# Performance work log

Hardware: AMD Instinct MI355X
Metric: run time of the kernel (lower is better)

## Reference

```python
import jax, jax.numpy as jnp
import numpy as np

BATCH, LENGTH, IN, STATE, OUT = 8, 4096, 512, 256, 512


def setup_inputs() -> dict:
    key = jax.random.key(0)
    k1, k2, k3, k4, k5 = jax.random.split(key, 5)
    u = jax.random.normal(k1, (BATCH, LENGTH, IN), dtype=jnp.float32)
    x0 = jax.random.normal(k2, (BATCH, STATE), dtype=jnp.float32)
    A = 0.9999 * (2.0 * jax.random.uniform(k3, (STATE,), dtype=jnp.float32) - 1.0)
    B = jax.random.normal(k4, (IN, STATE), dtype=jnp.float32) / (STATE + IN) ** 0.5
    C = jax.random.normal(k5, (STATE, OUT), dtype=jnp.float32) / STATE ** 0.5
    return {"u": u, "x0": x0, "A": A, "B": B, "C": C}


def reference(u, x0, A, B, C):
    L = u.shape[1]
    # A_powers[t, n] = A[n] ** t, shape [L, state]
    A_powers = jnp.power(A[None, :], jnp.arange(L, dtype=u.dtype)[:, None])
    uB = u @ B  # [batch, L, state]
    # FFT convolution; inputs are real so rfft/irfft gives same result as
    # real(ifft(fft*fft)) in the original.
    T = 2 ** int(np.ceil(np.log2(2 * L - 1)))
    Af = jnp.fft.rfft(A_powers, n=T, axis=0)  # [T/2+1, state]
    Uf = jnp.fft.rfft(uB, n=T, axis=1)        # [batch, T/2+1, state]
    x = jnp.fft.irfft(Af[None, :, :] * Uf, n=T, axis=1)[:, :L]  # [batch, L, state]
    # initial-state contribution: A * A_powers * x0
    x = x + A[None, None, :] * A_powers[None, :, :] * x0[:, None, :]
    y = x @ C  # [batch, L, out]
    return (y, x[:, -1])
```

## Files before the change

kernel.cpp:

```cpp
#include <hip/hip_runtime.h>

#define BATCH   8
#define LENGTH  4096
#define IN_DIM  512
#define STATE   256
#define OUT_DIM 512
#define NC      64
#define LC      64

typedef __attribute__((ext_vector_type(8))) short bf16x8;
typedef __attribute__((ext_vector_type(4))) float f32x4;

__device__ __forceinline__ unsigned short bf16_rne(float v) {
    unsigned u = __builtin_bit_cast(unsigned, v);
    unsigned r = (u + 0x7FFFu + ((u >> 16) & 1u)) >> 16;
    return (unsigned short)r;
}
__device__ __forceinline__ float bf16_f(unsigned short h) {
    unsigned u = ((unsigned)h) << 16;
    return __builtin_bit_cast(float, u);
}

__global__ __launch_bounds__(256) void split_u_kernel(
    const float* __restrict__ in, unsigned short* __restrict__ hi,
    unsigned short* __restrict__ lo)
{
    size_t i = ((size_t)blockIdx.x * 256 + threadIdx.x) * 4;
    float4 v = *(const float4*)(in + i);
    ushort4 h, l;
    h.x = bf16_rne(v.x); l.x = bf16_rne(v.x - bf16_f(h.x));
    h.y = bf16_rne(v.y); l.y = bf16_rne(v.y - bf16_f(h.y));
    h.z = bf16_rne(v.z); l.z = bf16_rne(v.z - bf16_f(h.z));
    h.w = bf16_rne(v.w); l.w = bf16_rne(v.w - bf16_f(h.w));
    *(ushort4*)(hi + i) = h;
    *(ushort4*)(lo + i) = l;
}

__global__ __launch_bounds__(256) void split_T_kernel(
    const float* __restrict__ in, unsigned short* __restrict__ hi,
    unsigned short* __restrict__ lo, int kbits, int Nsrc)
{
    int id = blockIdx.x * 256 + threadIdx.x;
    int k = id & ((1 << kbits) - 1);
    int n = id >> kbits;
    float v = in[(size_t)k * Nsrc + n];
    unsigned short h = bf16_rne(v);
    hi[id] = h;
    lo[id] = bf16_rne(v - bf16_f(h));
}

__global__ __launch_bounds__(256) void gemm_split(
    const unsigned short* __restrict__ Ahi, const unsigned short* __restrict__ Alo,
    const unsigned short* __restrict__ Bhi, const unsigned short* __restrict__ Blo,
    float* __restrict__ Cc, int N_, int K)
{
    __shared__ unsigned short lds[4 * 512 * 8];

    const int tid  = threadIdx.x;
    const int wave = tid >> 6;
    const int lane = tid & 63;
    const int n0 = blockIdx.x * 128;
    const int m0 = blockIdx.y * 128;

    const unsigned short* op =
        (wave == 0) ? Ahi : (wave == 1) ? Alo : (wave == 2) ? Bhi : Blo;
    const int rowBase = (wave < 2) ? m0 : n0;

    const unsigned short* g[8];
    #pragma unroll
    for (int i = 0; i < 8; ++i) {
        int p = i * 64 + lane;
        int row = p >> 2;
        int kg = (p & 3) ^ ((row >> 1) & 3);
        g[i] = op + (size_t)(rowBase + row) * K + kg * 8;
    }

    const int r = lane & 15, q = lane >> 4;
    const int wm = (wave >> 1) * 64, wn = (wave & 1) * 64;

    int aoff[4], boff[4];
    #pragma unroll
    for (int i = 0; i < 4; ++i) {
        int row = wm + i * 16 + r;
        aoff[i] = (row * 4 + (q ^ ((row >> 1) & 3))) * 8;
        row = wn + i * 16 + r;
        boff[i] = (row * 4 + (q ^ ((row >> 1) & 3))) * 8;
    }

    f32x4 acc[4][4];
    #pragma unroll
    for (int i = 0; i < 4; ++i)
        #pragma unroll
        for (int j = 0; j < 4; ++j)
            acc[i][j] = (f32x4){0.f, 0.f, 0.f, 0.f};

    for (int k0 = 0; k0 < K; k0 += 32) {
        #pragma unroll
        for (int i = 0; i < 8; ++i) {
            __builtin_amdgcn_global_load_lds(
                (const __attribute__((address_space(1))) unsigned int*)(g[i]),
                (__attribute__((address_space(3))) unsigned int*)(&lds[wave * 4096 + i * 512]),
                16, 0, 0);
            g[i] += 32;
        }
        __syncthreads();

        bf16x8 ahi[4], alo[4], bhi[4], blo[4];
        #pragma unroll
        for (int i = 0; i < 4; ++i) {
            ahi[i] = *(const bf16x8*)(&lds[        aoff[i]]);
            alo[i] = *(const bf16x8*)(&lds[ 4096 + aoff[i]]);
            bhi[i] = *(const bf16x8*)(&lds[ 8192 + boff[i]]);
            blo[i] = *(const bf16x8*)(&lds[12288 + boff[i]]);
        }
        #pragma unroll
        for (int i = 0; i < 4; ++i)
            #pragma unroll
            for (int j = 0; j < 4; ++j) {
                acc[i][j] = __builtin_amdgcn_mfma_f32_16x16x32_bf16(ahi[i], bhi[j], acc[i][j], 0, 0, 0);
                acc[i][j] = __builtin_amdgcn_mfma_f32_16x16x32_bf16(alo[i], bhi[j], acc[i][j], 0, 0, 0);
                acc[i][j] = __builtin_amdgcn_mfma_f32_16x16x32_bf16(ahi[i], blo[j], acc[i][j], 0, 0, 0);
            }
        __syncthreads();
    }

    #pragma unroll
    for (int i = 0; i < 4; ++i) {
        #pragma unroll
        for (int reg = 0; reg < 4; ++reg) {
            int mg = m0 + wm + i * 16 + q * 4 + reg;
            float* dst = Cc + (size_t)mg * N_ + n0 + wn + r;
            #pragma unroll
            for (int j = 0; j < 4; ++j)
                dst[j * 16] = acc[i][j][reg];
        }
    }
}

__global__ __launch_bounds__(256) void scan_carry(
    const float* __restrict__ uB, const float* __restrict__ A,
    float* __restrict__ carry)
{
    const int b = blockIdx.x;
    const int c = blockIdx.y;
    const int n = threadIdx.x;
    const float a = A[n];
    const float* p = uB + ((size_t)b * LENGTH + (size_t)c * LC) * STATE + n;
    float s = 0.f;
    #pragma unroll 8
    for (int j = 0; j < LC; ++j) s = a * s + p[(size_t)j * STATE];
    carry[((size_t)b * NC + c) * STATE + n] = s;
}

__global__ __launch_bounds__(256) void scan_combine(
    const float* __restrict__ carry, const float* __restrict__ A,
    const float* __restrict__ x0, float* __restrict__ h)
{
    const int b = blockIdx.x;
    const int n = threadIdx.x;
    const float a = A[n];
    float a2 = a * a, a4 = a2 * a2, a8 = a4 * a4, a16 = a8 * a8, a32 = a16 * a16;
    const float aLC = a32 * a32;
    float s = x0[(size_t)b * STATE + n];
    for (int c = 0; c < NC; ++c) {
        h[((size_t)b * NC + c) * STATE + n] = s;
        s = aLC * s + carry[((size_t)b * NC + c) * STATE + n];
    }
}

__global__ __launch_bounds__(256) void scan_apply(
    const float* __restrict__ uB, const float* __restrict__ A,
    const float* __restrict__ h, unsigned short* __restrict__ x_hi,
    unsigned short* __restrict__ x_lo, float* __restrict__ x_last)
{
    const int b = blockIdx.x;
    const int c = blockIdx.y;
    const int n = threadIdx.x;
    const float a = A[n];
    float s = h[((size_t)b * NC + c) * STATE + n];
    const size_t base = ((size_t)b * LENGTH + (size_t)c * LC) * STATE + n;
    const float* p = uB + base;
    #pragma unroll 4
    for (int j = 0; j < LC; ++j) {
        s = a * s + p[(size_t)j * STATE];
        unsigned short hh = bf16_rne(s);
        x_hi[base + (size_t)j * STATE] = hh;
        x_lo[base + (size_t)j * STATE] = bf16_rne(s - bf16_f(hh));
    }
    if (c == NC - 1) x_last[(size_t)b * STATE + n] = s;
}

extern "C" void kernel_launch(void* const* d_in, const int* in_sizes, int n_in,
                              void* d_out, int out_size, void* d_ws, size_t ws_size,
                              hipStream_t stream)
{
    const float* u  = (const float*)d_in[0];
    const float* x0 = (const float*)d_in[1];
    const float* A  = (const float*)d_in[2];
    const float* B  = (const float*)d_in[3];
    const float* C  = (const float*)d_in[4];

    const size_t MB = 1024 * 1024;
    char* ws = (char*)d_ws;

    unsigned short* u_hi = (unsigned short*)(ws);
    unsigned short* u_lo = (unsigned short*)(ws + 32 * MB);
    unsigned short* x_hi = (unsigned short*)(ws);
    unsigned short* x_lo = (unsigned short*)(ws + 16 * MB);
    float* carry = (float*)(ws + 64 * MB);
    float* h     = (float*)(ws + 64 * MB + 512 * 1024);
    unsigned short* Bt_hi = (unsigned short*)(ws + 65 * MB);
    unsigned short* Bt_lo = (unsigned short*)(ws + 65 * MB + 256 * 1024);
    unsigned short* Ct_hi = (unsigned short*)(ws + 65 * MB + 512 * 1024);
    unsigned short* Ct_lo = (unsigned short*)(ws + 65 * MB + 768 * 1024);

    float* y      = (float*)d_out;
    float* x_last = y + (size_t)BATCH * LENGTH * OUT_DIM;
    float* uB     = (float*)((char*)d_out + 32 * MB);

    const int M = BATCH * LENGTH;
    dim3 blk(256);

    split_u_kernel<<<dim3((M * IN_DIM) / 1024), blk, 0, stream>>>(u, u_hi, u_lo);
    split_T_kernel<<<dim3((IN_DIM * STATE) / 256), blk, 0, stream>>>(B, Bt_hi, Bt_lo, 9, STATE);
    split_T_kernel<<<dim3((STATE * OUT_DIM) / 256), blk, 0, stream>>>(C, Ct_hi, Ct_lo, 8, OUT_DIM);

    gemm_split<<<dim3(STATE / 128, M / 128), blk, 0, stream>>>(
        u_hi, u_lo, Bt_hi, Bt_lo, uB, STATE, IN_DIM);

    scan_carry  <<<dim3(BATCH, NC), blk, 0, stream>>>(uB, A, carry);
    scan_combine<<<dim3(BATCH),     blk, 0, stream>>>(carry, A, x0, h);
    scan_apply  <<<dim3(BATCH, NC), blk, 0, stream>>>(uB, A, h, x_hi, x_lo, x_last);

    gemm_split<<<dim3(OUT_DIM / 128, M / 128), blk, 0, stream>>>(
        x_hi, x_lo, Ct_hi, Ct_lo, y, OUT_DIM, STATE);
}
```

Before: 222.8 us.

## Split fp32 activations into bf16 hi/lo inside a double-buffered 512-thread GEMM

Removes the separate split_u pass and the bf16 hi/lo outputs of the scan. The GEMM now loads fp32 activations directly into LDS and splits them into hi/lo bf16 fragments in registers (the hi part is truncated rather than rounded). The GEMM also becomes a 512-thread, double-buffered kernel with a manual barrier/waitcnt pipeline. scan_combine is folded into scan_apply, where each chunk recomputes its prefix from the carries. This cuts HBM traffic and kernel launches, at the cost of redundant prefix work, more LDS, and extra conversion ALU inside the GEMM loop.

```diff
diff --git a/kernel.cpp b/kernel.cpp
--- a/kernel.cpp
+++ b/kernel.cpp
@@ -11,6 +11,8 @@
 typedef __attribute__((ext_vector_type(8))) short bf16x8;
 typedef __attribute__((ext_vector_type(4))) float f32x4;
 
+union FragU { bf16x8 v; unsigned u[4]; };
+
 __device__ __forceinline__ unsigned short bf16_rne(float v) {
     unsigned u = __builtin_bit_cast(unsigned, v);
     unsigned r = (u + 0x7FFFu + ((u >> 16) & 1u)) >> 16;
@@ -19,21 +21,6 @@
 __device__ __forceinline__ float bf16_f(unsigned short h) {
     unsigned u = ((unsigned)h) << 16;
     return __builtin_bit_cast(float, u);
-}
-
-__global__ __launch_bounds__(256) void split_u_kernel(
-    const float* __restrict__ in, unsigned short* __restrict__ hi,
-    unsigned short* __restrict__ lo)
-{
-    size_t i = ((size_t)blockIdx.x * 256 + threadIdx.x) * 4;
-    float4 v = *(const float4*)(in + i);
-    ushort4 h, l;
-    h.x = bf16_rne(v.x); l.x = bf16_rne(v.x - bf16_f(h.x));
-    h.y = bf16_rne(v.y); l.y = bf16_rne(v.y - bf16_f(h.y));
-    h.z = bf16_rne(v.z); l.z = bf16_rne(v.z - bf16_f(h.z));
-    h.w = bf16_rne(v.w); l.w = bf16_rne(v.w - bf16_f(h.w));
-    *(ushort4*)(hi + i) = h;
-    *(ushort4*)(lo + i) = l;
 }
 
 __global__ __launch_bounds__(256) void split_T_kernel(
@@ -49,12 +36,12 @@
     lo[id] = bf16_rne(v - bf16_f(h));
 }
 
-__global__ __launch_bounds__(256) void gemm_split(
-    const unsigned short* __restrict__ Ahi, const unsigned short* __restrict__ Alo,
-    const unsigned short* __restrict__ Bhi, const unsigned short* __restrict__ Blo,
-    float* __restrict__ Cc, int N_, int K)
-{
-    __shared__ unsigned short lds[4 * 512 * 8];
+__global__ __launch_bounds__(512, 4) void gemm_dbuf(
+    const float* __restrict__ Af, const unsigned short* __restrict__ Bthi,
+    const unsigned short* __restrict__ Btlo, float* __restrict__ Cc,
+    int N_, int K)
+{
+    __shared__ unsigned short lds[2 * 16384];
 
     const int tid  = threadIdx.x;
     const int wave = tid >> 6;
@@ -62,66 +49,125 @@
     const int n0 = blockIdx.x * 128;
     const int m0 = blockIdx.y * 128;
 
-    const unsigned short* op =
-        (wave == 0) ? Ahi : (wave == 1) ? Alo : (wave == 2) ? Bhi : Blo;
-    const int rowBase = (wave < 2) ? m0 : n0;
-
-    const unsigned short* g[8];
-    #pragma unroll
-    for (int i = 0; i < 8; ++i) {
-        int p = i * 64 + lane;
-        int row = p >> 2;
-        int kg = (p & 3) ^ ((row >> 1) & 3);
-        g[i] = op + (size_t)(rowBase + row) * K + kg * 8;
+    const char* gp[4];
+    int ldsoff[4], gstep[4];
+    #pragma unroll
+    for (int t = 0; t < 4; ++t) {
+        int gi = wave * 4 + t;
+        if (gi < 16) {
+            int p = gi * 64 + lane;
+            int row = p >> 3, s = p & 7;
+            int l = s ^ (row & 7);
+            gp[t] = (const char*)(Af + (size_t)(m0 + row) * K + l * 4);
+            gstep[t] = 32 * 4;
+            ldsoff[t] = gi * 512;
+        } else {
+            int q2 = (gi - 16) >> 3;
+            int pi = gi & 7;
+            int p = pi * 64 + lane;
+            int row = p >> 2, s = p & 3;
+            int l = s ^ ((row >> 1) & 3);
+            const unsigned short* base = q2 ? Btlo : Bthi;
+            gp[t] = (const char*)(base + (size_t)(n0 + row) * K + l * 8);
+            gstep[t] = 32 * 2;
+            ldsoff[t] = 8192 + q2 * 4096 + pi * 512;
+        }
     }
 
     const int r = lane & 15, q = lane >> 4;
-    const int wm = (wave >> 1) * 64, wn = (wave & 1) * 64;
-
-    int aoff[4], boff[4];
+    const int wm = (wave >> 2) * 64, wn = (wave & 3) * 32;
+
+    int aoff[4][2], boff[2];
     #pragma unroll
     for (int i = 0; i < 4; ++i) {
         int row = wm + i * 16 + r;
-        aoff[i] = (row * 4 + (q ^ ((row >> 1) & 3))) * 8;
-        row = wn + i * 16 + r;
-        boff[i] = (row * 4 + (q ^ ((row >> 1) & 3))) * 8;
-    }
-
-    f32x4 acc[4][4];
+        #pragma unroll
+        for (int h = 0; h < 2; ++h)
+            aoff[i][h] = row * 64 + ((2 * q + h) ^ (row & 7)) * 8;
+    }
+    #pragma unroll
+    for (int j = 0; j < 2; ++j) {
+        int row = wn + j * 16 + r;
+        boff[j] = row * 32 + (q ^ ((row >> 1) & 3)) * 8;
+    }
+
+    f32x4 acc[4][2];
     #pragma unroll
     for (int i = 0; i < 4; ++i)
         #pragma unroll
-        for (int j = 0; j < 4; ++j)
+        for (int j = 0; j < 2; ++j)
             acc[i][j] = (f32x4){0.f, 0.f, 0.f, 0.f};
 
-    for (int k0 = 0; k0 < K; k0 += 32) {
-        #pragma unroll
-        for (int i = 0; i < 8; ++i) {
-            __builtin_amdgcn_global_load_lds(
-                (const __attribute__((address_space(1))) unsigned int*)(g[i]),
-                (__attribute__((address_space(3))) unsigned int*)(&lds[wave * 4096 + i * 512]),
-                16, 0, 0);
-            g[i] += 32;
-        }
-        __syncthreads();
-
-        bf16x8 ahi[4], alo[4], bhi[4], blo[4];
+    #pragma unroll
+    for (int t = 0; t < 4; ++t) {
+        __builtin_amdgcn_global_load_lds(
+            (const __attribute__((address_space(1))) unsigned*)(gp[t]),
+            (__attribute__((address_space(3))) unsigned*)(&lds[ldsoff[t]]),
+            16, 0, 0);
+        gp[t] += gstep[t];
+    }
+
+    const int nit = K >> 5;
+    for (int it = 0; it < nit; ++it) {
+        asm volatile("" ::: "memory");
+        __builtin_amdgcn_s_barrier();
+        asm volatile("" ::: "memory");
+        if (it + 1 < nit) {
+            const int bb = ((it + 1) & 1) * 16384;
+            #pragma unroll
+            for (int t = 0; t < 4; ++t) {
+                __builtin_amdgcn_global_load_lds(
+                    (const __attribute__((address_space(1))) unsigned*)(gp[t]),
+                    (__attribute__((address_space(3))) unsigned*)(&lds[bb + ldsoff[t]]),
+                    16, 0, 0);
+                gp[t] += gstep[t];
+            }
+            __builtin_amdgcn_s_waitcnt(0x0F74);
+        } else {
+            __builtin_amdgcn_s_waitcnt(0x0F70);
+        }
+        asm volatile("" ::: "memory");
+        __builtin_amdgcn_s_barrier();
+        asm volatile("" ::: "memory");
+
+        const unsigned short* buf = &lds[(it & 1) * 16384];
+
+        FragU ahi[4], alo[4];
         #pragma unroll
         for (int i = 0; i < 4; ++i) {
-            ahi[i] = *(const bf16x8*)(&lds[        aoff[i]]);
-            alo[i] = *(const bf16x8*)(&lds[ 4096 + aoff[i]]);
-            bhi[i] = *(const bf16x8*)(&lds[ 8192 + boff[i]]);
-            blo[i] = *(const bf16x8*)(&lds[12288 + boff[i]]);
+            #pragma unroll
+            for (int h = 0; h < 2; ++h) {
+                float4 f = *(const float4*)(buf + aoff[i][h]);
+                unsigned bx = __builtin_bit_cast(unsigned, f.x);
+                unsigned by = __builtin_bit_cast(unsigned, f.y);
+                unsigned bz = __builtin_bit_cast(unsigned, f.z);
+                unsigned bw = __builtin_bit_cast(unsigned, f.w);
+                ahi[i].u[h * 2]     = __builtin_amdgcn_perm(by, bx, 0x07060302);
+                ahi[i].u[h * 2 + 1] = __builtin_amdgcn_perm(bw, bz, 0x07060302);
+                float lx = f.x - __builtin_bit_cast(float, bx & 0xFFFF0000u);
+                float ly = f.y - __builtin_bit_cast(float, by & 0xFFFF0000u);
+                float lz = f.z - __builtin_bit_cast(float, bz & 0xFFFF0000u);
+                float lw = f.w - __builtin_bit_cast(float, bw & 0xFFFF0000u);
+                alo[i].u[h * 2]     = __builtin_amdgcn_perm(
+                    __builtin_bit_cast(unsigned, ly), __builtin_bit_cast(unsigned, lx), 0x07060302);
+                alo[i].u[h * 2 + 1] = __builtin_amdgcn_perm(
+                    __builtin_bit_cast(unsigned, lw), __builtin_bit_cast(unsigned, lz), 0x07060302);
+            }
+        }
+        FragU bhi[2], blo[2];
+        #pragma unroll
+        for (int j = 0; j < 2; ++j) {
+            bhi[j].v = *(const bf16x8*)(buf +  8192 + boff[j]);
+            blo[j].v = *(const bf16x8*)(buf + 12288 + boff[j]);
         }
         #pragma unroll
         for (int i = 0; i < 4; ++i)
             #pragma unroll
-            for (int j = 0; j < 4; ++j) {
-                acc[i][j] = __builtin_amdgcn_mfma_f32_16x16x32_bf16(ahi[i], bhi[j], acc[i][j], 0, 0, 0);
-                acc[i][j] = __builtin_amdgcn_mfma_f32_16x16x32_bf16(alo[i], bhi[j], acc[i][j], 0, 0, 0);
-                acc[i][j] = __builtin_amdgcn_mfma_f32_16x16x32_bf16(ahi[i], blo[j], acc[i][j], 0, 0, 0);
+            for (int j = 0; j < 2; ++j) {
+                acc[i][j] = __builtin_amdgcn_mfma_f32_16x16x32_bf16(ahi[i].v, bhi[j].v, acc[i][j], 0, 0, 0);
+                acc[i][j] = __builtin_amdgcn_mfma_f32_16x16x32_bf16(alo[i].v, bhi[j].v, acc[i][j], 0, 0, 0);
+                acc[i][j] = __builtin_amdgcn_mfma_f32_16x16x32_bf16(ahi[i].v, blo[j].v, acc[i][j], 0, 0, 0);
             }
-        __syncthreads();
     }
 
     #pragma unroll
@@ -130,9 +176,8 @@
         for (int reg = 0; reg < 4; ++reg) {
             int mg = m0 + wm + i * 16 + q * 4 + reg;
             float* dst = Cc + (size_t)mg * N_ + n0 + wn + r;
-            #pragma unroll
-            for (int j = 0; j < 4; ++j)
-                dst[j * 16] = acc[i][j][reg];
+            dst[0]  = acc[i][0][reg];
+            dst[16] = acc[i][1][reg];
         }
     }
 }
@@ -152,40 +197,29 @@
     carry[((size_t)b * NC + c) * STATE + n] = s;
 }
 
-__global__ __launch_bounds__(256) void scan_combine(
-    const float* __restrict__ carry, const float* __restrict__ A,
-    const float* __restrict__ x0, float* __restrict__ h)
+__global__ __launch_bounds__(256) void scan_apply(
+    const float* __restrict__ uB, const float* __restrict__ A,
+    const float* __restrict__ carry, const float* __restrict__ x0,
+    float* __restrict__ x, float* __restrict__ x_last)
 {
     const int b = blockIdx.x;
+    const int c = blockIdx.y;
     const int n = threadIdx.x;
     const float a = A[n];
     float a2 = a * a, a4 = a2 * a2, a8 = a4 * a4, a16 = a8 * a8, a32 = a16 * a16;
     const float aLC = a32 * a32;
+
     float s = x0[(size_t)b * STATE + n];
-    for (int c = 0; c < NC; ++c) {
-        h[((size_t)b * NC + c) * STATE + n] = s;
-        s = aLC * s + carry[((size_t)b * NC + c) * STATE + n];
-    }
-}
-
-__global__ __launch_bounds__(256) void scan_apply(
-    const float* __restrict__ uB, const float* __restrict__ A,
-    const float* __restrict__ h, unsigned short* __restrict__ x_hi,
-    unsigned short* __restrict__ x_lo, float* __restrict__ x_last)
-{
-    const int b = blockIdx.x;
-    const int c = blockIdx.y;
-    const int n = threadIdx.x;
-    const float a = A[n];
-    float s = h[((size_t)b * NC + c) * STATE + n];
+    for (int d = 0; d < c; ++d)
+        s = aLC * s + carry[((size_t)b * NC + d) * STATE + n];
+
     const size_t base = ((size_t)b * LENGTH + (size_t)c * LC) * STATE + n;
     const float* p = uB + base;
-    #pragma unroll 4
+    float* qx = x + base;
+    #pragma unroll 8
     for (int j = 0; j < LC; ++j) {
         s = a * s + p[(size_t)j * STATE];
-        unsigned short hh = bf16_rne(s);
-        x_hi[base + (size_t)j * STATE] = hh;
-        x_lo[base + (size_t)j * STATE] = bf16_rne(s - bf16_f(hh));
+        qx[(size_t)j * STATE] = s;
     }
     if (c == NC - 1) x_last[(size_t)b * STATE + n] = s;
 }
@@ -203,35 +237,28 @@
     const size_t MB = 1024 * 1024;
     char* ws = (char*)d_ws;
 
-    unsigned short* u_hi = (unsigned short*)(ws);
-    unsigned short* u_lo = (unsigned short*)(ws + 32 * MB);
-    unsigned short* x_hi = (unsigned short*)(ws);
-    unsigned short* x_lo = (unsigned short*)(ws + 16 * MB);
-    float* carry = (float*)(ws + 64 * MB);
-    float* h     = (float*)(ws + 64 * MB + 512 * 1024);
-    unsigned short* Bt_hi = (unsigned short*)(ws + 65 * MB);
-    unsigned short* Bt_lo = (unsigned short*)(ws + 65 * MB + 256 * 1024);
-    unsigned short* Ct_hi = (unsigned short*)(ws + 65 * MB + 512 * 1024);
-    unsigned short* Ct_lo = (unsigned short*)(ws + 65 * MB + 768 * 1024);
+    float* x     = (float*)(ws);
+    float* carry = (float*)(ws + 32 * MB);
+    unsigned short* Bt_hi = (unsigned short*)(ws + 33 * MB);
+    unsigned short* Bt_lo = (unsigned short*)(ws + 33 * MB + 256 * 1024);
+    unsigned short* Ct_hi = (unsigned short*)(ws + 33 * MB + 512 * 1024);
+    unsigned short* Ct_lo = (unsigned short*)(ws + 33 * MB + 768 * 1024);
 
     float* y      = (float*)d_out;
     float* x_last = y + (size_t)BATCH * LENGTH * OUT_DIM;
     float* uB     = (float*)((char*)d_out + 32 * MB);
 
     const int M = BATCH * LENGTH;
-    dim3 blk(256);
-
-    split_u_kernel<<<dim3((M * IN_DIM) / 1024), blk, 0, stream>>>(u, u_hi, u_lo);
-    split_T_kernel<<<dim3((IN_DIM * STATE) / 256), blk, 0, stream>>>(B, Bt_hi, Bt_lo, 9, STATE);
-    split_T_kernel<<<dim3((STATE * OUT_DIM) / 256), blk, 0, stream>>>(C, Ct_hi, Ct_lo, 8, OUT_DIM);
-
-    gemm_split<<<dim3(STATE / 128, M / 128), blk, 0, stream>>>(
-        u_hi, u_lo, Bt_hi, Bt_lo, uB, STATE, IN_DIM);
-
-    scan_carry  <<<dim3(BATCH, NC), blk, 0, stream>>>(uB, A, carry);
-    scan_combine<<<dim3(BATCH),     blk, 0, stream>>>(carry, A, x0, h);
-    scan_apply  <<<dim3(BATCH, NC), blk, 0, stream>>>(uB, A, h, x_hi, x_lo, x_last);
-
-    gemm_split<<<dim3(OUT_DIM / 128, M / 128), blk, 0, stream>>>(
-        x_hi, x_lo, Ct_hi, Ct_lo, y, OUT_DIM, STATE);
-}
+
+    split_T_kernel<<<dim3((IN_DIM * STATE) / 256), dim3(256), 0, stream>>>(B, Bt_hi, Bt_lo, 9, STATE);
+    split_T_kernel<<<dim3((STATE * OUT_DIM) / 256), dim3(256), 0, stream>>>(C, Ct_hi, Ct_lo, 8, OUT_DIM);
+
+    gemm_dbuf<<<dim3(STATE / 128, M / 128), dim3(512), 0, stream>>>(
+        u, Bt_hi, Bt_lo, uB, STATE, IN_DIM);
+
+    scan_carry<<<dim3(BATCH, NC), dim3(256), 0, stream>>>(uB, A, carry);
+    scan_apply<<<dim3(BATCH, NC), dim3(256), 0, stream>>>(uB, A, carry, x0, x, x_last);
+
+    gemm_dbuf<<<dim3(OUT_DIM / 128, M / 128), dim3(512), 0, stream>>>(
+        x, Ct_hi, Ct_lo, y, OUT_DIM, STATE);
+}
```

Result: faster. 209.2 us (-6.1%).
